# Kernel optimization log

Measured on AMD Instinct MI355X. Metric: run time of the kernel, lower is better.

Reference implementation:

```python
import jax, jax.numpy as jnp
import numpy as np


def _extract_patch_points(x, p):
    # x: (n, c, h, w) -> (n, c*p*p, h*w) patch feature vectors (edge-padded),
    # matching build_extended_map + build_pts_set_for_flann ordering.
    n, c, h, w = x.shape
    step = p // 2
    y = jnp.pad(x, ((0, 0), (0, 0), (step, step), (step, step)), mode='edge')
    shifts = [y[:, :, i:i + h, j:j + w] for i in range(p) for j in range(p)]
    feat = jnp.stack(shifts, axis=2)            # (n, c, p*p, h, w)
    return feat.reshape(n, c * p * p, h * w)    # (n, d, hw)


def setup_inputs() -> dict:
    key = jax.random.key(0)
    k1, k2 = jax.random.split(key)
    source_map = jax.random.normal(k1, (1, 32, 128, 128), dtype=jnp.float32)
    target_map = jax.random.normal(k2, (1, 32, 128, 128), dtype=jnp.float32)
    return {"source_map": source_map, "target_map": target_map, "patch_size": 3}


def reference(source_map, target_map, patch_size):
    n, c, sh, sw = source_map.shape
    tw = target_map.shape[3]
    pts = _extract_patch_points(target_map, patch_size)   # (n, d, Np)
    q_pts = _extract_patch_points(source_map, patch_size) # (n, d, Nq)

    def nn_one(p_feat, q_feat):
        p = p_feat.T  # (Np, d) target points
        q = q_feat.T  # (Nq, d) query points
        r_p = jnp.sum(p * p, axis=1, keepdims=True)   # (Np, 1)
        r_q = jnp.sum(q * q, axis=1, keepdims=True)   # (Nq, 1)
        mul = q @ p.T                                  # (Nq, Np)
        # Faithful to original pairwise_dist (its r_p/r_q broadcast orientation
        # requires Np == Nq, which holds here):
        dist = r_p - 2.0 * mul + r_q.T                 # (Nq, Np)
        return jnp.argmin(dist, axis=1), jnp.min(dist, axis=1)

    nn_idx, nnd = jax.vmap(nn_one)(pts, q_pts)         # (n, Nq) each
    idy = nn_idx // tw
    idx = nn_idx % tw
    nnf = jnp.stack([idy.reshape(n, sh, sw), idx.reshape(n, sh, sw)], axis=1).astype(jnp.int32)
    nnd = nnd.reshape(n, 1, sh, sw)
    return nnf, nnd
```

## Files before the change

### kernel.cpp

```cpp
#include <hip/hip_runtime.h>
#include <stdint.h>

#define NPT   16384
#define KE    64
#define ROWB  8192

typedef _Float16 f16;
typedef __attribute__((ext_vector_type(8))) _Float16 half8;
typedef __attribute__((ext_vector_type(4))) float floatx4;

#define AS1(p) ((const __attribute__((address_space(1))) uint32_t*)(p))
#define AS3(p) ((__attribute__((address_space(3))) uint32_t*)(p))

__global__ __launch_bounds__(256)
void extract_kernel(const float* __restrict__ src, const float* __restrict__ tgt,
                    f16* __restrict__ Aext, f16* __restrict__ Bext,
                    double* __restrict__ n2s, double* __restrict__ n2t) {
  __shared__ f16 bufA[256 * KE];
  __shared__ f16 bufB[256 * KE];
  const int tid = threadIdx.x;
  const int pt = blockIdx.x * 256 + tid;
  double sA = 0.0, sB = 0.0;
#pragma unroll
  for (int c = 0; c < 32; ++c) {
    float v = src[(c << 14) + pt];
    sA += (double)v * (double)v;
    f16 h = (f16)v;
    bufA[tid * KE + c] = h;
    bufA[tid * KE + 32 + c] = (f16)(v - (float)h);
    v = tgt[(c << 14) + pt];
    sB += (double)v * (double)v;
    h = (f16)v;
    bufB[tid * KE + c] = h;
    bufB[tid * KE + 32 + c] = (f16)(v - (float)h);
  }
  n2s[pt] = sA;
  n2t[pt] = sB;
  __syncthreads();
  const uint4* s4A = (const uint4*)bufA;
  const uint4* s4B = (const uint4*)bufB;
  uint4* gA = (uint4*)(Aext + (size_t)blockIdx.x * 256 * KE);
  uint4* gB = (uint4*)(Bext + (size_t)blockIdx.x * 256 * KE);
#pragma unroll
  for (int it = 0; it < 8; ++it) {
    gA[it * 256 + tid] = s4A[it * 256 + tid];
    gB[it * 256 + tid] = s4B[it * 256 + tid];
  }
}

__global__ __launch_bounds__(256)
void norm_blur_kernel(const double* __restrict__ n2s, const double* __restrict__ n2t,
                      float* __restrict__ rq, float* __restrict__ rp,
                      unsigned long long* __restrict__ best) {
  const int pt = blockIdx.x * 256 + threadIdx.x;
  const int y = pt >> 7, x = pt & 127;
  double sq = 0.0, sp_ = 0.0;
#pragma unroll
  for (int dy = -1; dy <= 1; ++dy) {
    int yy = y + dy; yy = yy < 0 ? 0 : (yy > 127 ? 127 : yy);
#pragma unroll
    for (int dx = -1; dx <= 1; ++dx) {
      int xx = x + dx; xx = xx < 0 ? 0 : (xx > 127 ? 127 : xx);
      sq  += n2s[(yy << 7) + xx];
      sp_ += n2t[(yy << 7) + xx];
    }
  }
  rq[pt] = (float)sq;
  rp[pt] = (float)sp_;
  best[pt] = 0xFFFFFFFFFFFFFFFFULL;
}

__global__ __launch_bounds__(512, 4)
void gemm_blur_argmin_kernel(const f16* __restrict__ A, const f16* __restrict__ B,
                             const float* __restrict__ rq,
                             unsigned long long* __restrict__ best) {
  __shared__ __align__(16) char smem[65536];
  f16* As0 = (f16*)smem;
  f16* Bs0 = (f16*)(smem + 16384);
  f16* As1 = (f16*)(smem + 32768);
  f16* Bs1 = (f16*)(smem + 49152);
  float* Cf = (float*)smem;

  const int L  = blockIdx.x;
  const int st = L >> 7;
  const int r  = L & 127;
  const int bx = ((st & 15) << 3) | (r & 7);
  const int by = ((st >> 4) << 4) | (r >> 3);
  const int yq = by;
  const int vt = bx;

  const int ym = __builtin_amdgcn_readfirstlane(yq > 0 ? yq - 1 : 0);
  const int yc = __builtin_amdgcn_readfirstlane(yq);
  const int yp = __builtin_amdgcn_readfirstlane(yq < 127 ? yq + 1 : 127);
  const int vm = __builtin_amdgcn_readfirstlane(vt > 0 ? vt - 1 : 0);
  const int vc = __builtin_amdgcn_readfirstlane(vt);
  const int vp = __builtin_amdgcn_readfirstlane(vt < 127 ? vt + 1 : 127);

  const int t = threadIdx.x;
  const int w = t >> 6;
  const int l = t & 63;

  const int lr = l >> 3;
  const int lt = l & 7;
  const int sl = lt ^ (lr & 7);
  int rowOff[2];
  rowOff[0] = (w * 16 + lr) * KE + sl * 8;
  rowOff[1] = rowOff[0] + 8 * KE;

#define STAGEW(Arow, Brow, Ad, Bd)                                             \
  { const f16* Ag = A + (size_t)(Arow) * ROWB;                                 \
    const f16* Bg = B + (size_t)(Brow) * ROWB;                                 \
    __builtin_amdgcn_global_load_lds(AS1(Ag + rowOff[0]),                      \
                                     AS3(&Ad[(w * 16) * 64]), 16, 0, 0);       \
    __builtin_amdgcn_global_load_lds(AS1(Ag + rowOff[1]),                      \
                                     AS3(&Ad[(w * 16 + 8) * 64]), 16, 0, 0);   \
    __builtin_amdgcn_global_load_lds(AS1(Bg + rowOff[0]),                      \
                                     AS3(&Bd[(w * 16) * 64]), 16, 0, 0);       \
    __builtin_amdgcn_global_load_lds(AS1(Bg + rowOff[1]),                      \
                                     AS3(&Bd[(w * 16 + 8) * 64]), 16, 0, 0); }

  const int m16 = l & 15;
  const int q   = l >> 4;
  const int pHi = q ^ (m16 & 7);
  const int pLo = pHi ^ 4;
  const int wRow = (w & 1) * 64;
  const int wCol = (w >> 1) * 32;
  const int aHiOff = m16 * 64 + pHi * 8;
  const int aLoOff = m16 * 64 + pLo * 8;

  floatx4 acc[4][2] = {};

#define COMPUTEW(Asb, Bsb)                                                     \
  { half8 ah[4], al[4];                                                        \
    _Pragma("unroll") for (int i = 0; i < 4; ++i) {                            \
      ah[i] = *(const half8*)&Asb[(wRow + i * 16) * 64 + aHiOff];              \
      al[i] = *(const half8*)&Asb[(wRow + i * 16) * 64 + aLoOff];              \
    }                                                                          \
    _Pragma("unroll") for (int j = 0; j < 2; ++j) {                            \
      half8 bh = *(const half8*)&Bsb[(wCol + j * 16) * 64 + aHiOff];           \
      _Pragma("unroll") for (int i = 0; i < 4; ++i)                            \
        acc[i][j] = __builtin_amdgcn_mfma_f32_16x16x32_f16(ah[i], bh, acc[i][j], 0, 0, 0); \
      _Pragma("unroll") for (int i = 0; i < 4; ++i)                            \
        acc[i][j] = __builtin_amdgcn_mfma_f32_16x16x32_f16(al[i], bh, acc[i][j], 0, 0, 0); \
    }                                                                          \
    _Pragma("unroll") for (int j = 0; j < 2; ++j) {                            \
      half8 bl = *(const half8*)&Bsb[(wCol + j * 16) * 64 + aLoOff];           \
      _Pragma("unroll") for (int i = 0; i < 4; ++i)                            \
        acc[i][j] = __builtin_amdgcn_mfma_f32_16x16x32_f16(ah[i], bl, acc[i][j], 0, 0, 0); \
    } }

  STAGEW(ym, vm, As0, Bs0);
  STAGEW(yc, vc, As1, Bs1);
  asm volatile("s_waitcnt vmcnt(4)" ::: "memory");
  __builtin_amdgcn_s_barrier();
  COMPUTEW(As0, Bs0);
  __builtin_amdgcn_s_barrier();
  STAGEW(yp, vp, As0, Bs0);
  asm volatile("s_waitcnt vmcnt(4)" ::: "memory");
  __builtin_amdgcn_s_barrier();
  COMPUTEW(As1, Bs1);
  asm volatile("s_waitcnt vmcnt(0)" ::: "memory");
  __builtin_amdgcn_s_barrier();
  COMPUTEW(As0, Bs0);
  __builtin_amdgcn_s_barrier();

#define SWZ(row, col) (((row) << 7) + ((((col) >> 2) ^ ((row) & 7)) << 2) + ((col) & 3))
#define LDCF(row, g) (*(const floatx4*)&Cf[((row) << 7) + ((((g) ^ ((row) & 7))) << 2)])

  const int xr_l = t >> 3;
  const int uo = t & 7;
  const int g0 = uo << 2;
  const floatx4* rq4 = (const floatx4*)(rq + (vt << 7));

#pragma unroll
  for (int ph = 0; ph < 2; ++ph) {
    if ((ph == 0) ? (wRow == 0) : (wRow == 64)) {
      const int rbase = ph;
#pragma unroll
      for (int i = 0; i < 4; ++i)
#pragma unroll
        for (int j = 0; j < 2; ++j) {
          const int col = wCol + j * 16 + m16;
#pragma unroll
          for (int r2 = 0; r2 < 4; ++r2) {
            const int lrow = rbase + i * 16 + q * 4 + r2;
            Cf[SWZ(lrow, col)] = acc[i][j][r2];
          }
        }
    } else if ((ph == 0) ? (q == 0) : (q == 3)) {
      const int lrow = ph ? 0 : 64;
#pragma unroll
      for (int j = 0; j < 2; ++j) {
        const int col = wCol + j * 16 + m16;
        Cf[SWZ(lrow, col)] = ph ? acc[3][j][3] : acc[0][j][0];
      }
    }
    __syncthreads();

    const int x   = ph * 64 + xr_l;
    const int lx  = ph ? xr_l + 1 : xr_l;
    const int lxm = ph ? lx - 1 : (xr_l ? xr_l - 1 : 0);
    const int lxp = (ph && x == 127) ? lx : lx + 1;

    float bf = __builtin_huge_valf();
    int bu = 0;
    float am_last = (uo == 0) ? LDCF(lxm, 0)[0] : LDCF(lxm, g0 - 1)[3];
    floatx4 Ap = LDCF(lxp, g0);
#pragma unroll
    for (int k = 0; k < 4; ++k) {
      const int g = g0 + k;
      const floatx4 Am = LDCF(lxm, g);
      const floatx4 Ac = LDCF(lx, g);
      floatx4 ApN = Ap;
      float ap4;
      if (k < 3)       { ApN = LDCF(lxp, g + 1); ap4 = ApN[0]; }
      else if (uo < 7) { ap4 = LDCF(lxp, g + 1)[0]; }
      else             { ap4 = Ap[3]; }
      const floatx4 rv = rq4[g];
      float o0 = am_last + Ac[0] + Ap[1];
      float o1 = Am[0]   + Ac[1] + Ap[2];
      float o2 = Am[1]   + Ac[2] + Ap[3];
      float o3 = Am[2]   + Ac[3] + ap4;
      am_last = Am[3];
      Ap = ApN;
      const int ub = g << 2;
      float f0 = fmaf(-2.0f, o0, rv[0]); if (f0 < bf) { bf = f0; bu = ub; }
      float f1 = fmaf(-2.0f, o1, rv[1]); if (f1 < bf) { bf = f1; bu = ub + 1; }
      float f2 = fmaf(-2.0f, o2, rv[2]); if (f2 < bf) { bf = f2; bu = ub + 2; }
      float f3 = fmaf(-2.0f, o3, rv[3]); if (f3 < bf) { bf = f3; bu = ub + 3; }
    }
    unsigned int bits = __float_as_uint(bf);
    unsigned int key = (bits & 0x80000000u) ? ~bits : (bits | 0x80000000u);
    unsigned long long pk =
        ((unsigned long long)key << 32) | (unsigned)((vt << 7) + bu);
    unsigned long long o1v = __shfl_xor(pk, 1); pk = pk < o1v ? pk : o1v;
    unsigned long long o2v = __shfl_xor(pk, 2); pk = pk < o2v ? pk : o2v;
    unsigned long long o4v = __shfl_xor(pk, 4); pk = pk < o4v ? pk : o4v;
    if (uo == 0) atomicMin(best + (yq << 7) + x, pk);
    if (ph == 0) __syncthreads();
  }
#undef SWZ
#undef LDCF
}

__global__ void finalize_kernel(const unsigned long long* __restrict__ best,
                                const float* __restrict__ rp,
                                float* __restrict__ out) {
  int i = blockIdx.x * 256 + threadIdx.x;
  if (i >= NPT) return;
  unsigned long long v = best[i];
  unsigned int col = (unsigned int)(v & 0xFFFFFFFFu);
  unsigned int key = (unsigned int)(v >> 32);
  unsigned int bits = (key & 0x80000000u) ? (key & 0x7FFFFFFFu) : ~key;
  float fmin = __uint_as_float(bits);
  out[i]           = (float)(col >> 7);
  out[NPT + i]     = (float)(col & 127);
  out[2 * NPT + i] = rp[i] + fmin;
}

extern "C" void kernel_launch(void* const* d_in, const int* in_sizes, int n_in,
                              void* d_out, int out_size, void* d_ws, size_t ws_size,
                              hipStream_t stream) {
  const float* src = (const float*)d_in[0];
  const float* tgt = (const float*)d_in[1];
  float* out = (float*)d_out;

  char* ws = (char*)d_ws;
  f16* Aext = (f16*)(ws);
  f16* Bext = (f16*)(ws + 2097152);
  double* n2s = (double*)(ws + 4194304);
  double* n2t = (double*)(ws + 4325376);
  float* rq = (float*)(ws + 4456448);
  float* rp = (float*)(ws + 4521984);
  unsigned long long* best = (unsigned long long*)(ws + 4587520);

  extract_kernel<<<64, 256, 0, stream>>>(src, tgt, Aext, Bext, n2s, n2t);
  norm_blur_kernel<<<64, 256, 0, stream>>>(n2s, n2t, rq, rp, best);
  gemm_blur_argmin_kernel<<<16384, 512, 0, stream>>>(Aext, Bext, rq, best);
  finalize_kernel<<<NPT / 256, 256, 0, stream>>>(best, rp, out);
}
```

Before: 305.1 us.

## Double GEMM block to 1024 threads and compute blur-argmin epilogue in one pass

The fused GEMM/blur/argmin kernel now launches 16 waves per block instead of 8. Each wave computes a 32x32 output tile instead of 64x32. Staging is split so half the waves load A and the other half load B. Because the full 128x128 fp32 result tile now fits in the 64KB shared buffer, the epilogue runs in a single pass instead of the previous two-phase write/sync/argmin loop, which needed halo-row handling. The aim is more waves in flight and fewer barriers. The risk is that the aggressive `__launch_bounds__(1024, 8)` forces tighter register limits or spills, and that LDS use still caps residency at a few blocks per CU.

```diff
diff --git a/kernel.cpp b/kernel.cpp
--- a/kernel.cpp
+++ b/kernel.cpp
@@ -70,7 +70,7 @@
   best[pt] = 0xFFFFFFFFFFFFFFFFULL;
 }
 
-__global__ __launch_bounds__(512, 4)
+__global__ __launch_bounds__(1024, 8)
 void gemm_blur_argmin_kernel(const f16* __restrict__ A, const f16* __restrict__ B,
                              const float* __restrict__ rq,
                              unsigned long long* __restrict__ best) {
@@ -103,60 +103,60 @@
   const int lr = l >> 3;
   const int lt = l & 7;
   const int sl = lt ^ (lr & 7);
-  int rowOff[2];
-  rowOff[0] = (w * 16 + lr) * KE + sl * 8;
-  rowOff[1] = rowOff[0] + 8 * KE;
-
-#define STAGEW(Arow, Brow, Ad, Bd)                                             \
-  { const f16* Ag = A + (size_t)(Arow) * ROWB;                                 \
-    const f16* Bg = B + (size_t)(Brow) * ROWB;                                 \
-    __builtin_amdgcn_global_load_lds(AS1(Ag + rowOff[0]),                      \
-                                     AS3(&Ad[(w * 16) * 64]), 16, 0, 0);       \
-    __builtin_amdgcn_global_load_lds(AS1(Ag + rowOff[1]),                      \
-                                     AS3(&Ad[(w * 16 + 8) * 64]), 16, 0, 0);   \
-    __builtin_amdgcn_global_load_lds(AS1(Bg + rowOff[0]),                      \
-                                     AS3(&Bd[(w * 16) * 64]), 16, 0, 0);       \
-    __builtin_amdgcn_global_load_lds(AS1(Bg + rowOff[1]),                      \
-                                     AS3(&Bd[(w * 16 + 8) * 64]), 16, 0, 0); }
+  const f16* Mg = (w < 8) ? A : B;
+  const int wr0 = (w < 8) ? ym : vm;
+  const int wr1 = (w < 8) ? yc : vc;
+  const int wr2 = (w < 8) ? yp : vp;
+  const int rowOff0 = ((w & 7) * 16 + lr) * KE + sl * 8;
+  const int rowOff1 = rowOff0 + 8 * KE;
+  const int ldsBase0 = ((w & 7) * 16) * 64;
+
+#define STAGE2(row, Ad, Bd)                                                    \
+  { const f16* g_ = Mg + (size_t)(row) * ROWB;                                 \
+    f16* d_ = (w < 8) ? (Ad) : (Bd);                                           \
+    __builtin_amdgcn_global_load_lds(AS1(g_ + rowOff0),                        \
+                                     AS3(d_ + ldsBase0), 16, 0, 0);            \
+    __builtin_amdgcn_global_load_lds(AS1(g_ + rowOff1),                        \
+                                     AS3(d_ + ldsBase0 + 8 * 64), 16, 0, 0); }
 
   const int m16 = l & 15;
   const int q   = l >> 4;
   const int pHi = q ^ (m16 & 7);
   const int pLo = pHi ^ 4;
-  const int wRow = (w & 1) * 64;
-  const int wCol = (w >> 1) * 32;
+  const int wRow = (w & 3) * 32;
+  const int wCol = (w >> 2) * 32;
   const int aHiOff = m16 * 64 + pHi * 8;
   const int aLoOff = m16 * 64 + pLo * 8;
 
-  floatx4 acc[4][2] = {};
+  floatx4 acc[2][2] = {};
 
 #define COMPUTEW(Asb, Bsb)                                                     \
-  { half8 ah[4], al[4];                                                        \
-    _Pragma("unroll") for (int i = 0; i < 4; ++i) {                            \
+  { half8 ah[2], al[2];                                                        \
+    _Pragma("unroll") for (int i = 0; i < 2; ++i) {                            \
       ah[i] = *(const half8*)&Asb[(wRow + i * 16) * 64 + aHiOff];              \
       al[i] = *(const half8*)&Asb[(wRow + i * 16) * 64 + aLoOff];              \
     }                                                                          \
     _Pragma("unroll") for (int j = 0; j < 2; ++j) {                            \
       half8 bh = *(const half8*)&Bsb[(wCol + j * 16) * 64 + aHiOff];           \
-      _Pragma("unroll") for (int i = 0; i < 4; ++i)                            \
+      _Pragma("unroll") for (int i = 0; i < 2; ++i)                            \
         acc[i][j] = __builtin_amdgcn_mfma_f32_16x16x32_f16(ah[i], bh, acc[i][j], 0, 0, 0); \
-      _Pragma("unroll") for (int i = 0; i < 4; ++i)                            \
+      _Pragma("unroll") for (int i = 0; i < 2; ++i)                            \
         acc[i][j] = __builtin_amdgcn_mfma_f32_16x16x32_f16(al[i], bh, acc[i][j], 0, 0, 0); \
     }                                                                          \
     _Pragma("unroll") for (int j = 0; j < 2; ++j) {                            \
       half8 bl = *(const half8*)&Bsb[(wCol + j * 16) * 64 + aLoOff];           \
-      _Pragma("unroll") for (int i = 0; i < 4; ++i)                            \
+      _Pragma("unroll") for (int i = 0; i < 2; ++i)                            \
         acc[i][j] = __builtin_amdgcn_mfma_f32_16x16x32_f16(ah[i], bl, acc[i][j], 0, 0, 0); \
     } }
 
-  STAGEW(ym, vm, As0, Bs0);
-  STAGEW(yc, vc, As1, Bs1);
-  asm volatile("s_waitcnt vmcnt(4)" ::: "memory");
+  STAGE2(wr0, As0, Bs0);
+  STAGE2(wr1, As1, Bs1);
+  asm volatile("s_waitcnt vmcnt(2)" ::: "memory");
   __builtin_amdgcn_s_barrier();
   COMPUTEW(As0, Bs0);
   __builtin_amdgcn_s_barrier();
-  STAGEW(yp, vp, As0, Bs0);
-  asm volatile("s_waitcnt vmcnt(4)" ::: "memory");
+  STAGE2(wr2, As0, Bs0);
+  asm volatile("s_waitcnt vmcnt(2)" ::: "memory");
   __builtin_amdgcn_s_barrier();
   COMPUTEW(As1, Bs1);
   asm volatile("s_waitcnt vmcnt(0)" ::: "memory");
@@ -167,78 +167,61 @@
 #define SWZ(row, col) (((row) << 7) + ((((col) >> 2) ^ ((row) & 7)) << 2) + ((col) & 3))
 #define LDCF(row, g) (*(const floatx4*)&Cf[((row) << 7) + ((((g) ^ ((row) & 7))) << 2)])
 
-  const int xr_l = t >> 3;
+#pragma unroll
+  for (int i = 0; i < 2; ++i)
+#pragma unroll
+    for (int j = 0; j < 2; ++j) {
+      const int col = wCol + j * 16 + m16;
+#pragma unroll
+      for (int r2 = 0; r2 < 4; ++r2) {
+        const int row = wRow + i * 16 + q * 4 + r2;
+        Cf[SWZ(row, col)] = acc[i][j][r2];
+      }
+    }
+  __syncthreads();
+
+  const int xr = t >> 3;
   const int uo = t & 7;
   const int g0 = uo << 2;
+  const int xm = xr > 0 ? xr - 1 : 0;
+  const int xp = xr < 127 ? xr + 1 : 127;
   const floatx4* rq4 = (const floatx4*)(rq + (vt << 7));
 
-#pragma unroll
-  for (int ph = 0; ph < 2; ++ph) {
-    if ((ph == 0) ? (wRow == 0) : (wRow == 64)) {
-      const int rbase = ph;
-#pragma unroll
-      for (int i = 0; i < 4; ++i)
-#pragma unroll
-        for (int j = 0; j < 2; ++j) {
-          const int col = wCol + j * 16 + m16;
-#pragma unroll
-          for (int r2 = 0; r2 < 4; ++r2) {
-            const int lrow = rbase + i * 16 + q * 4 + r2;
-            Cf[SWZ(lrow, col)] = acc[i][j][r2];
-          }
-        }
-    } else if ((ph == 0) ? (q == 0) : (q == 3)) {
-      const int lrow = ph ? 0 : 64;
-#pragma unroll
-      for (int j = 0; j < 2; ++j) {
-        const int col = wCol + j * 16 + m16;
-        Cf[SWZ(lrow, col)] = ph ? acc[3][j][3] : acc[0][j][0];
-      }
-    }
-    __syncthreads();
-
-    const int x   = ph * 64 + xr_l;
-    const int lx  = ph ? xr_l + 1 : xr_l;
-    const int lxm = ph ? lx - 1 : (xr_l ? xr_l - 1 : 0);
-    const int lxp = (ph && x == 127) ? lx : lx + 1;
-
-    float bf = __builtin_huge_valf();
-    int bu = 0;
-    float am_last = (uo == 0) ? LDCF(lxm, 0)[0] : LDCF(lxm, g0 - 1)[3];
-    floatx4 Ap = LDCF(lxp, g0);
-#pragma unroll
-    for (int k = 0; k < 4; ++k) {
-      const int g = g0 + k;
-      const floatx4 Am = LDCF(lxm, g);
-      const floatx4 Ac = LDCF(lx, g);
-      floatx4 ApN = Ap;
-      float ap4;
-      if (k < 3)       { ApN = LDCF(lxp, g + 1); ap4 = ApN[0]; }
-      else if (uo < 7) { ap4 = LDCF(lxp, g + 1)[0]; }
-      else             { ap4 = Ap[3]; }
-      const floatx4 rv = rq4[g];
-      float o0 = am_last + Ac[0] + Ap[1];
-      float o1 = Am[0]   + Ac[1] + Ap[2];
-      float o2 = Am[1]   + Ac[2] + Ap[3];
-      float o3 = Am[2]   + Ac[3] + ap4;
-      am_last = Am[3];
-      Ap = ApN;
-      const int ub = g << 2;
-      float f0 = fmaf(-2.0f, o0, rv[0]); if (f0 < bf) { bf = f0; bu = ub; }
-      float f1 = fmaf(-2.0f, o1, rv[1]); if (f1 < bf) { bf = f1; bu = ub + 1; }
-      float f2 = fmaf(-2.0f, o2, rv[2]); if (f2 < bf) { bf = f2; bu = ub + 2; }
-      float f3 = fmaf(-2.0f, o3, rv[3]); if (f3 < bf) { bf = f3; bu = ub + 3; }
-    }
-    unsigned int bits = __float_as_uint(bf);
-    unsigned int key = (bits & 0x80000000u) ? ~bits : (bits | 0x80000000u);
-    unsigned long long pk =
-        ((unsigned long long)key << 32) | (unsigned)((vt << 7) + bu);
-    unsigned long long o1v = __shfl_xor(pk, 1); pk = pk < o1v ? pk : o1v;
-    unsigned long long o2v = __shfl_xor(pk, 2); pk = pk < o2v ? pk : o2v;
-    unsigned long long o4v = __shfl_xor(pk, 4); pk = pk < o4v ? pk : o4v;
-    if (uo == 0) atomicMin(best + (yq << 7) + x, pk);
-    if (ph == 0) __syncthreads();
-  }
+  float bf = __builtin_huge_valf();
+  int bu = 0;
+  float am_last = (uo == 0) ? LDCF(xm, 0)[0] : LDCF(xm, g0 - 1)[3];
+  floatx4 Ap = LDCF(xp, g0);
+#pragma unroll
+  for (int k = 0; k < 4; ++k) {
+    const int g = g0 + k;
+    const floatx4 Am = LDCF(xm, g);
+    const floatx4 Ac = LDCF(xr, g);
+    floatx4 ApN = Ap;
+    float ap4;
+    if (k < 3)       { ApN = LDCF(xp, g + 1); ap4 = ApN[0]; }
+    else if (uo < 7) { ap4 = LDCF(xp, g + 1)[0]; }
+    else             { ap4 = Ap[3]; }
+    const floatx4 rv = rq4[g];
+    float o0 = am_last + Ac[0] + Ap[1];
+    float o1 = Am[0]   + Ac[1] + Ap[2];
+    float o2 = Am[1]   + Ac[2] + Ap[3];
+    float o3 = Am[2]   + Ac[3] + ap4;
+    am_last = Am[3];
+    Ap = ApN;
+    const int ub = g << 2;
+    float f0 = fmaf(-2.0f, o0, rv[0]); if (f0 < bf) { bf = f0; bu = ub; }
+    float f1 = fmaf(-2.0f, o1, rv[1]); if (f1 < bf) { bf = f1; bu = ub + 1; }
+    float f2 = fmaf(-2.0f, o2, rv[2]); if (f2 < bf) { bf = f2; bu = ub + 2; }
+    float f3 = fmaf(-2.0f, o3, rv[3]); if (f3 < bf) { bf = f3; bu = ub + 3; }
+  }
+  unsigned int bits = __float_as_uint(bf);
+  unsigned int key = (bits & 0x80000000u) ? ~bits : (bits | 0x80000000u);
+  unsigned long long pk =
+      ((unsigned long long)key << 32) | (unsigned)((vt << 7) + bu);
+  unsigned long long o1v = __shfl_xor(pk, 1); pk = pk < o1v ? pk : o1v;
+  unsigned long long o2v = __shfl_xor(pk, 2); pk = pk < o2v ? pk : o2v;
+  unsigned long long o4v = __shfl_xor(pk, 4); pk = pk < o4v ? pk : o4v;
+  if (uo == 0) atomicMin(best + (yq << 7) + xr, pk);
 #undef SWZ
 #undef LDCF
 }
@@ -276,6 +259,6 @@
 
   extract_kernel<<<64, 256, 0, stream>>>(src, tgt, Aext, Bext, n2s, n2t);
   norm_blur_kernel<<<64, 256, 0, stream>>>(n2s, n2t, rq, rp, best);
-  gemm_blur_argmin_kernel<<<16384, 512, 0, stream>>>(Aext, Bext, rq, best);
+  gemm_blur_argmin_kernel<<<16384, 1024, 0, stream>>>(Aext, Bext, rq, best);
   finalize_kernel<<<NPT / 256, 256, 0, stream>>>(best, rp, out);
 }
```

Result: slower. 366.7 us (+20.2%).

## Single-buffer B tile and shrink LDS to raise GEMM kernel occupancy

Applied to the files above, without the earlier changes.

Shared memory drops from 64KB to 48KB by keeping two A buffers but only one B buffer, so the B tile for each step is reloaded only after the previous compute finishes. The MFMA inner loop is restructured to hold only two A fragment pairs at a time, cutting register pressure, and launch bounds are raised from 4 to 6 to allow more resident blocks. The aim is higher occupancy to hide latency. The cost is that B loads now serialize with compute, since the B stage can no longer overlap the previous step's MFMAs.

```diff
diff --git a/kernel.cpp b/kernel.cpp
--- a/kernel.cpp
+++ b/kernel.cpp
@@ -70,15 +70,14 @@
   best[pt] = 0xFFFFFFFFFFFFFFFFULL;
 }
 
-__global__ __launch_bounds__(512, 4)
+__global__ __launch_bounds__(512, 6)
 void gemm_blur_argmin_kernel(const f16* __restrict__ A, const f16* __restrict__ B,
                              const float* __restrict__ rq,
                              unsigned long long* __restrict__ best) {
-  __shared__ __align__(16) char smem[65536];
-  f16* As0 = (f16*)smem;
-  f16* Bs0 = (f16*)(smem + 16384);
-  f16* As1 = (f16*)(smem + 32768);
-  f16* Bs1 = (f16*)(smem + 49152);
+  __shared__ __align__(16) char smem[49152];
+  f16* A0 = (f16*)smem;
+  f16* A1 = (f16*)(smem + 16384);
+  f16* Bs = (f16*)(smem + 32768);
   float* Cf = (float*)smem;
 
   const int L  = blockIdx.x;
@@ -103,21 +102,19 @@
   const int lr = l >> 3;
   const int lt = l & 7;
   const int sl = lt ^ (lr & 7);
-  int rowOff[2];
-  rowOff[0] = (w * 16 + lr) * KE + sl * 8;
-  rowOff[1] = rowOff[0] + 8 * KE;
-
-#define STAGEW(Arow, Brow, Ad, Bd)                                             \
-  { const f16* Ag = A + (size_t)(Arow) * ROWB;                                 \
-    const f16* Bg = B + (size_t)(Brow) * ROWB;                                 \
-    __builtin_amdgcn_global_load_lds(AS1(Ag + rowOff[0]),                      \
-                                     AS3(&Ad[(w * 16) * 64]), 16, 0, 0);       \
-    __builtin_amdgcn_global_load_lds(AS1(Ag + rowOff[1]),                      \
-                                     AS3(&Ad[(w * 16 + 8) * 64]), 16, 0, 0);   \
-    __builtin_amdgcn_global_load_lds(AS1(Bg + rowOff[0]),                      \
-                                     AS3(&Bd[(w * 16) * 64]), 16, 0, 0);       \
-    __builtin_amdgcn_global_load_lds(AS1(Bg + rowOff[1]),                      \
-                                     AS3(&Bd[(w * 16 + 8) * 64]), 16, 0, 0); }
+  const int rowOff0 = (w * 16 + lr) * KE + sl * 8;
+  const int rowOff1 = rowOff0 + 8 * KE;
+  const int ldsOff0 = (w * 16) * 64;
+  const int ldsOff1 = (w * 16 + 8) * 64;
+
+#define STAGE_A(row, Ad)                                                       \
+  { const f16* g_ = A + (size_t)(row) * ROWB;                                  \
+    __builtin_amdgcn_global_load_lds(AS1(g_ + rowOff0), AS3((Ad) + ldsOff0), 16, 0, 0); \
+    __builtin_amdgcn_global_load_lds(AS1(g_ + rowOff1), AS3((Ad) + ldsOff1), 16, 0, 0); }
+#define STAGE_B(row)                                                           \
+  { const f16* g_ = B + (size_t)(row) * ROWB;                                  \
+    __builtin_amdgcn_global_load_lds(AS1(g_ + rowOff0), AS3(Bs + ldsOff0), 16, 0, 0); \
+    __builtin_amdgcn_global_load_lds(AS1(g_ + rowOff1), AS3(Bs + ldsOff1), 16, 0, 0); }
 
   const int m16 = l & 15;
   const int q   = l >> 4;
@@ -130,39 +127,44 @@
 
   floatx4 acc[4][2] = {};
 
-#define COMPUTEW(Asb, Bsb)                                                     \
-  { half8 ah[4], al[4];                                                        \
-    _Pragma("unroll") for (int i = 0; i < 4; ++i) {                            \
-      ah[i] = *(const half8*)&Asb[(wRow + i * 16) * 64 + aHiOff];              \
-      al[i] = *(const half8*)&Asb[(wRow + i * 16) * 64 + aLoOff];              \
-    }                                                                          \
-    _Pragma("unroll") for (int j = 0; j < 2; ++j) {                            \
-      half8 bh = *(const half8*)&Bsb[(wCol + j * 16) * 64 + aHiOff];           \
-      _Pragma("unroll") for (int i = 0; i < 4; ++i)                            \
-        acc[i][j] = __builtin_amdgcn_mfma_f32_16x16x32_f16(ah[i], bh, acc[i][j], 0, 0, 0); \
-      _Pragma("unroll") for (int i = 0; i < 4; ++i)                            \
-        acc[i][j] = __builtin_amdgcn_mfma_f32_16x16x32_f16(al[i], bh, acc[i][j], 0, 0, 0); \
-    }                                                                          \
-    _Pragma("unroll") for (int j = 0; j < 2; ++j) {                            \
-      half8 bl = *(const half8*)&Bsb[(wCol + j * 16) * 64 + aLoOff];           \
-      _Pragma("unroll") for (int i = 0; i < 4; ++i)                            \
-        acc[i][j] = __builtin_amdgcn_mfma_f32_16x16x32_f16(ah[i], bl, acc[i][j], 0, 0, 0); \
+#define COMPUTEW(Asb)                                                          \
+  { _Pragma("unroll") for (int ih = 0; ih < 2; ++ih) {                         \
+      half8 ah0 = *(const half8*)&(Asb)[(wRow + ih * 32) * 64 + aHiOff];       \
+      half8 ah1 = *(const half8*)&(Asb)[(wRow + ih * 32 + 16) * 64 + aHiOff];  \
+      half8 al0 = *(const half8*)&(Asb)[(wRow + ih * 32) * 64 + aLoOff];       \
+      half8 al1 = *(const half8*)&(Asb)[(wRow + ih * 32 + 16) * 64 + aLoOff];  \
+      _Pragma("unroll") for (int j = 0; j < 2; ++j) {                          \
+        half8 bh = *(const half8*)&Bs[(wCol + j * 16) * 64 + aHiOff];          \
+        acc[ih*2+0][j] = __builtin_amdgcn_mfma_f32_16x16x32_f16(ah0, bh, acc[ih*2+0][j], 0, 0, 0); \
+        acc[ih*2+1][j] = __builtin_amdgcn_mfma_f32_16x16x32_f16(ah1, bh, acc[ih*2+1][j], 0, 0, 0); \
+        acc[ih*2+0][j] = __builtin_amdgcn_mfma_f32_16x16x32_f16(al0, bh, acc[ih*2+0][j], 0, 0, 0); \
+        acc[ih*2+1][j] = __builtin_amdgcn_mfma_f32_16x16x32_f16(al1, bh, acc[ih*2+1][j], 0, 0, 0); \
+      }                                                                        \
+      _Pragma("unroll") for (int j = 0; j < 2; ++j) {                          \
+        half8 bl = *(const half8*)&Bs[(wCol + j * 16) * 64 + aLoOff];          \
+        acc[ih*2+0][j] = __builtin_amdgcn_mfma_f32_16x16x32_f16(ah0, bl, acc[ih*2+0][j], 0, 0, 0); \
+        acc[ih*2+1][j] = __builtin_amdgcn_mfma_f32_16x16x32_f16(ah1, bl, acc[ih*2+1][j], 0, 0, 0); \
+      }                                                                        \
     } }
 
-  STAGEW(ym, vm, As0, Bs0);
-  STAGEW(yc, vc, As1, Bs1);
-  asm volatile("s_waitcnt vmcnt(4)" ::: "memory");
-  __builtin_amdgcn_s_barrier();
-  COMPUTEW(As0, Bs0);
-  __builtin_amdgcn_s_barrier();
-  STAGEW(yp, vp, As0, Bs0);
-  asm volatile("s_waitcnt vmcnt(4)" ::: "memory");
-  __builtin_amdgcn_s_barrier();
-  COMPUTEW(As1, Bs1);
+  STAGE_A(ym, A0);
+  STAGE_B(vm);
+  STAGE_A(yc, A1);
+  asm volatile("s_waitcnt vmcnt(2)" ::: "memory");
+  __builtin_amdgcn_s_barrier();
+  COMPUTEW(A0);
+  __builtin_amdgcn_s_barrier();
+  STAGE_B(vc);
+  STAGE_A(yp, A0);
+  asm volatile("s_waitcnt vmcnt(2)" ::: "memory");
+  __builtin_amdgcn_s_barrier();
+  COMPUTEW(A1);
+  __builtin_amdgcn_s_barrier();
+  STAGE_B(vp);
   asm volatile("s_waitcnt vmcnt(0)" ::: "memory");
   __builtin_amdgcn_s_barrier();
-  COMPUTEW(As0, Bs0);
-  __builtin_amdgcn_s_barrier();
+  COMPUTEW(A0);
+  __syncthreads();
 
 #define SWZ(row, col) (((row) << 7) + ((((col) >> 2) ^ ((row) & 7)) << 2) + ((col) & 3))
 #define LDCF(row, g) (*(const floatx4*)&Cf[((row) << 7) + ((((g) ^ ((row) & 7))) << 2)])
```

New measurement: 641.7 us. +110.3%, slower.
